# Performance work log

Measured on AMD Instinct MI355X. Metric: run time of the kernel, lower is better.

The kernel has to match this reference:

```python
import jax, jax.numpy as jnp
import numpy as np

HEAD_DIM = 128
N_HEADS = 32
N_KV = 8
EPS = 1e-6


def setup_inputs() -> dict:
    key = jax.random.key(0)
    ks = jax.random.split(key, 8)
    B, S, H = 1, 2048, 2560
    hidden_states = jax.random.normal(ks[0], (B, S, H), dtype=jnp.float32)
    # rotary embeddings (any values work for a math reference)
    pos = jnp.arange(S, dtype=jnp.float32)[:, None]
    inv_freq = 1.0 / (10000.0 ** (jnp.arange(0, HEAD_DIM, 2, dtype=jnp.float32) / HEAD_DIM))
    ang = pos * inv_freq[None, :]            # [S, HEAD_DIM/2]
    emb = jnp.concatenate([ang, ang], axis=-1)  # [S, HEAD_DIM]
    cos = jnp.cos(emb)[None]                 # [1, S, HEAD_DIM]
    sin = jnp.sin(emb)[None]
    sc = 0.02
    Wq = jax.random.normal(ks[1], (N_HEADS * HEAD_DIM, H), dtype=jnp.float32) * sc
    Wk = jax.random.normal(ks[2], (N_KV * HEAD_DIM, H), dtype=jnp.float32) * sc
    Wv = jax.random.normal(ks[3], (N_KV * HEAD_DIM, H), dtype=jnp.float32) * sc
    Wo = jax.random.normal(ks[4], (H, N_HEADS * HEAD_DIM), dtype=jnp.float32) * sc
    q_norm_w = jnp.ones((HEAD_DIM,), dtype=jnp.float32)
    k_norm_w = jnp.ones((HEAD_DIM,), dtype=jnp.float32)
    return dict(hidden_states=hidden_states, cos=cos, sin=sin,
                Wq=Wq, Wk=Wk, Wv=Wv, Wo=Wo,
                q_norm_w=q_norm_w, k_norm_w=k_norm_w)


def _rms_norm(x, w):
    var = jnp.mean(x * x, axis=-1, keepdims=True)
    return x * jax.lax.rsqrt(var + EPS) * w


def _rotate_half(x):
    x1, x2 = jnp.split(x, 2, axis=-1)
    return jnp.concatenate([-x2, x1], axis=-1)


def reference(hidden_states, cos, sin, Wq, Wk, Wv, Wo, q_norm_w, k_norm_w):
    B, S, H = hidden_states.shape
    scale = HEAD_DIM ** -0.5
    # projections -> [B, heads, S, D]
    q = (hidden_states @ Wq.T).reshape(B, S, N_HEADS, HEAD_DIM)
    k = (hidden_states @ Wk.T).reshape(B, S, N_KV, HEAD_DIM)
    v = (hidden_states @ Wv.T).reshape(B, S, N_KV, HEAD_DIM)
    q = _rms_norm(q, q_norm_w).transpose(0, 2, 1, 3)   # [B, 32, S, D]
    k = _rms_norm(k, k_norm_w).transpose(0, 2, 1, 3)   # [B, 8, S, D]
    v = v.transpose(0, 2, 1, 3)
    # RoPE (cos/sin broadcast over heads via [:, None])
    c = cos[:, None]
    s = sin[:, None]
    q = q * c + _rotate_half(q) * s
    k = k * c + _rotate_half(k) * s
    # GQA: expand kv heads (repeat_kv)
    rep = N_HEADS // N_KV
    k = jnp.repeat(k, rep, axis=1)  # [B, 32, S, D]
    v = jnp.repeat(v, rep, axis=1)
    # causal SDPA (prefill => is_causal=True, full-length cache)
    scores = jnp.einsum('bhqd,bhkd->bhqk', q, k) * scale
    causal = jnp.tril(jnp.ones((S, S), dtype=bool))
    scores = jnp.where(causal, scores, jnp.finfo(scores.dtype).min)
    probs = jax.nn.softmax(scores, axis=-1)
    out = jnp.einsum('bhqk,bhkd->bhqd', probs, v)      # [B, 32, S, D]
    out = out.transpose(0, 2, 1, 3).reshape(B, S, N_HEADS * HEAD_DIM)
    return out @ Wo.T
```

## Files before the change

### kernel.cpp

```cpp
#include <hip/hip_runtime.h>
#include <hip/hip_bf16.h>

#define S_LEN   2048
#define HID     2560
#define NH      32
#define NKV     8
#define HD      128
#define QDIM    (NH*HD)
#define KVDIM   (NKV*HD)

typedef __attribute__((ext_vector_type(8))) short short8;
typedef __attribute__((ext_vector_type(4))) float f32x4;

__device__ __forceinline__ unsigned short f2bf(float f) {
    unsigned u = __float_as_uint(f);
    u += 0x7fffu + ((u >> 16) & 1u);
    return (unsigned short)(u >> 16);
}
__device__ __forceinline__ float bf2f(unsigned short s) {
    return __uint_as_float(((unsigned)s) << 16);
}
__device__ __forceinline__ unsigned pk2bf(float a, float b) {
    __hip_bfloat162 h = __float22bfloat162_rn(make_float2(a, b));
    union { __hip_bfloat162 h; unsigned u; } c; c.h = h; return c.u;
}
__device__ __forceinline__ void gload16(const void* g, void* l) {
    __builtin_amdgcn_global_load_lds(
        (const __attribute__((address_space(1))) unsigned int*)g,
        (__attribute__((address_space(3))) unsigned int*)l, 16, 0, 0);
}

#define N4_HS  (S_LEN*HID/4)
#define N4_WQ  (QDIM*HID/4)
#define N4_WKV (KVDIM*HID/4)
__global__ __launch_bounds__(256) void cvt4(
    const float* __restrict__ hs, const float* __restrict__ Wq,
    const float* __restrict__ Wk, const float* __restrict__ Wv,
    unsigned short* __restrict__ hsB, unsigned short* __restrict__ WqB,
    unsigned short* __restrict__ WkB, unsigned short* __restrict__ WvB)
{
    int i = blockIdx.x * 256 + threadIdx.x;
    const float* s; unsigned short* d;
    if (i < N4_HS)                          { s = hs; d = hsB; }
    else if (i < N4_HS + N4_WQ)             { i -= N4_HS; s = Wq; d = WqB; }
    else if (i < N4_HS + N4_WQ + N4_WKV)    { i -= N4_HS + N4_WQ; s = Wk; d = WkB; }
    else                                    { i -= N4_HS + N4_WQ + N4_WKV; s = Wv; d = WvB; }
    float4 v = ((const float4*)s)[i];
    uint2 o;
    o.x = pk2bf(v.x, v.y); o.y = pk2bf(v.z, v.w);
    ((uint2*)d)[i] = o;
}

__global__ __launch_bounds__(256) void cvt_f32_bf16(
    const float* __restrict__ s, unsigned short* __restrict__ d, int n4)
{
    int i = blockIdx.x * 256 + threadIdx.x;
    if (i >= n4) return;
    float4 v = ((const float4*)s)[i];
    uint2 o;
    o.x = pk2bf(v.x, v.y); o.y = pk2bf(v.z, v.w);
    ((uint2*)d)[i] = o;
}

struct GemmRegs {
    f32x4 acc[4][4];
};
__device__ __forceinline__ void gemm_core(
    const unsigned short* A, const unsigned short* B, int Kd,
    unsigned short* As, unsigned short* Bs, GemmRegs& R,
    int rowA0, int rowB0, int tid)
{
    const int lane = tid & 63;
    const int l15 = lane & 15, l4 = lane >> 4;
    const int w = tid >> 6;
    const int wr = (w >> 1) * 64, wc = (w & 1) * 64;
    const int sw = l15 & 7;

#pragma unroll
    for (int i = 0; i < 4; i++)
#pragma unroll
        for (int j = 0; j < 4; j++)
            R.acc[i][j] = (f32x4){0.f, 0.f, 0.f, 0.f};

    for (int k0 = 0; k0 < Kd; k0 += 64) {
        __syncthreads();
#pragma unroll
        for (int i = 0; i < 4; i++) {
            int tc = tid + i * 256;
            int r = tc >> 3, cl = tc & 7;
            int cg = cl ^ (r & 7);
            gload16(A + (size_t)(rowA0 + r) * Kd + k0 + cg * 8, &As[tc * 8]);
            gload16(B + (size_t)(rowB0 + r) * Kd + k0 + cg * 8, &Bs[tc * 8]);
        }
        __syncthreads();

#pragma unroll
        for (int ks = 0; ks < 2; ks++) {
            const int kc = (ks * 4 + l4) ^ sw;
            short8 af[4], bf[4];
#pragma unroll
            for (int i = 0; i < 4; i++)
                af[i] = *(const short8*)&As[(wr + i*16 + l15)*64 + kc*8];
#pragma unroll
            for (int j = 0; j < 4; j++)
                bf[j] = *(const short8*)&Bs[(wc + j*16 + l15)*64 + kc*8];
#pragma unroll
            for (int i = 0; i < 4; i++)
#pragma unroll
                for (int j = 0; j < 4; j++)
                    R.acc[i][j] = __builtin_amdgcn_mfma_f32_16x16x32_bf16(
                        af[i], bf[j], R.acc[i][j], 0, 0, 0);
        }
    }
}

__global__ __launch_bounds__(256) void gemm_qkv(
    const unsigned short* __restrict__ A,
    const unsigned short* __restrict__ Wq, const unsigned short* __restrict__ Wk,
    const unsigned short* __restrict__ Wv,
    unsigned short* __restrict__ Qo, unsigned short* __restrict__ Ko,
    unsigned short* __restrict__ VTo)
{
    __shared__ unsigned short As[128*64];
    __shared__ unsigned short Bs[128*64];
    const int bx = blockIdx.x;
    const unsigned short* B;
    if (bx < 32)      B = Wq + (size_t)bx*128*HID;
    else if (bx < 40) B = Wk + (size_t)(bx-32)*128*HID;
    else              B = Wv + (size_t)(bx-40)*128*HID;

    const int tid = threadIdx.x;
    const int lane = tid & 63, w = tid >> 6;
    const int l15 = lane & 15, l4 = lane >> 4;
    const int wr = (w >> 1) * 64, wc = (w & 1) * 64;
    GemmRegs R;
    gemm_core(A, B, HID, As, Bs, R, blockIdx.y * 128, 0, tid);

    if (bx < 40) {
        unsigned short* C; int ldc, cb;
        if (bx < 32) { C = Qo; ldc = QDIM;  cb = bx*128; }
        else         { C = Ko; ldc = KVDIM; cb = (bx-32)*128; }
#pragma unroll
        for (int i = 0; i < 4; i++)
#pragma unroll
            for (int j = 0; j < 4; j++) {
                int row0 = blockIdx.y*128 + wr + i*16 + l4*4;
                int col  = cb + wc + j*16 + l15;
#pragma unroll
                for (int r = 0; r < 4; r++)
                    C[(size_t)(row0 + r) * ldc + col] = f2bf(R.acc[i][j][r]);
            }
    } else {
        const int cbase = (bx - 40) * 128;
#pragma unroll
        for (int i = 0; i < 4; i++)
#pragma unroll
            for (int j = 0; j < 4; j++) {
                int col  = cbase + wc + j*16 + l15;
                int row0 = blockIdx.y*128 + wr + i*16 + l4*4;
                int kvhh = col >> 7, d = col & 127;
                unsigned short* p = VTo + (size_t)kvhh*HD*S_LEN + (size_t)d*S_LEN + row0;
                uint2 pk;
                pk.x = pk2bf(R.acc[i][j][0], R.acc[i][j][1]);
                pk.y = pk2bf(R.acc[i][j][2], R.acc[i][j][3]);
                *(uint2*)p = pk;
            }
    }
}

__global__ __launch_bounds__(256) void gemm_out(
    const unsigned short* __restrict__ A, const unsigned short* __restrict__ B,
    float* __restrict__ C, int N, int Kd)
{
    __shared__ unsigned short As[64*64];
    __shared__ unsigned short Bs[160*64];
    const int tid = threadIdx.x;
    const int lane = tid & 63, w = tid >> 6;
    const int l15 = lane & 15, l4 = lane >> 4;
    const int wr = (w >> 1) * 32, wc = (w & 1) * 80;
    const int rowA0 = blockIdx.y * 64, rowB0 = blockIdx.x * 160;
    const int sw = l15 & 7;

    f32x4 acc[2][5];
#pragma unroll
    for (int i = 0; i < 2; i++)
#pragma unroll
        for (int j = 0; j < 5; j++) acc[i][j] = (f32x4){0.f, 0.f, 0.f, 0.f};

    for (int k0 = 0; k0 < Kd; k0 += 64) {
        __syncthreads();
#pragma unroll
        for (int i = 0; i < 2; i++) {
            int tc = tid + i * 256;
            int r = tc >> 3, cl = tc & 7;
            int cg = cl ^ (r & 7);
            gload16(A + (size_t)(rowA0 + r) * Kd + k0 + cg * 8, &As[tc * 8]);
        }
#pragma unroll
        for (int i = 0; i < 5; i++) {
            int tc = tid + i * 256;
            int r = tc >> 3, cl = tc & 7;
            int cg = cl ^ (r & 7);
            gload16(B + (size_t)(rowB0 + r) * Kd + k0 + cg * 8, &Bs[tc * 8]);
        }
        __syncthreads();

#pragma unroll
        for (int ks = 0; ks < 2; ks++) {
            const int kc = (ks * 4 + l4) ^ sw;
            short8 af[2], bf[5];
#pragma unroll
            for (int i = 0; i < 2; i++)
                af[i] = *(const short8*)&As[(wr + i*16 + l15)*64 + kc*8];
#pragma unroll
            for (int j = 0; j < 5; j++)
                bf[j] = *(const short8*)&Bs[(wc + j*16 + l15)*64 + kc*8];
#pragma unroll
            for (int i = 0; i < 2; i++)
#pragma unroll
                for (int j = 0; j < 5; j++)
                    acc[i][j] = __builtin_amdgcn_mfma_f32_16x16x32_bf16(
                        af[i], bf[j], acc[i][j], 0, 0, 0);
        }
    }

#pragma unroll
    for (int i = 0; i < 2; i++)
#pragma unroll
        for (int j = 0; j < 5; j++) {
            int row0 = rowA0 + wr + i*16 + l4*4;
            int col  = rowB0 + wc + j*16 + l15;
#pragma unroll
            for (int r = 0; r < 4; r++)
                C[(size_t)(row0 + r) * N + col] = acc[i][j][r];
        }
}

__global__ __launch_bounds__(256) void rmsnorm_rope_all(
    unsigned short* __restrict__ Qx, unsigned short* __restrict__ Kx,
    const float* __restrict__ qw, const float* __restrict__ kw,
    const float* __restrict__ ct, const float* __restrict__ st)
{
    int wid  = (blockIdx.x * blockDim.x + threadIdx.x) >> 6;
    int lane = threadIdx.x & 63;
    unsigned short* x; const float* w; int s;
    if (wid < S_LEN * NH) {
        int h = wid & (NH - 1); s = wid >> 5;
        x = Qx + (size_t)s * QDIM + h * HD; w = qw;
    } else {
        wid -= S_LEN * NH;
        int h = wid & (NKV - 1); s = wid >> 3;
        x = Kx + (size_t)s * KVDIM + h * HD; w = kw;
    }

    float x1 = bf2f(x[lane]);
    float x2 = bf2f(x[lane + 64]);
    float ss = x1*x1 + x2*x2;
#pragma unroll
    for (int off = 32; off > 0; off >>= 1) ss += __shfl_xor(ss, off, 64);
    float r = rsqrtf(ss * (1.0f/128.0f) + 1e-6f);
    float n1 = x1 * r * w[lane];
    float n2 = x2 * r * w[lane + 64];
    float c1 = ct[s*HD + lane],      s1 = st[s*HD + lane];
    float c2 = ct[s*HD + lane + 64], s2 = st[s*HD + lane + 64];
    x[lane]      = f2bf(n1*c1 - n2*s1);
    x[lane + 64] = f2bf(n2*c2 + n1*s2);
}

__global__ __launch_bounds__(256, 3) void flash_mfma(
    const unsigned short* __restrict__ Q, const unsigned short* __restrict__ K,
    const unsigned short* __restrict__ VT, unsigned short* __restrict__ O)
{
    const int bid = blockIdx.x;
    const int kvh = bid & 7;
    const int h   = kvh * 4 + ((bid >> 3) & 3);
    const int pb  = bid >> 5;
    const int tid = threadIdx.x;
    const int w = tid >> 6, lane = tid & 63;
    const int l15 = lane & 15, l4 = lane >> 4;

    __shared__ unsigned short Ks[64*128];
    __shared__ unsigned short Vt[128*64];
    __shared__ unsigned short Ps[4*16*72];
    __shared__ float Lw[4][16];

    const float scale2 = 0.08838834764831845f * 1.4426950408889634f;
    const float M2 = 17.3f;
    unsigned short* Pw = &Ps[w * 16 * 72];
    const unsigned short* VTh = VT + (size_t)kvh * HD * S_LEN;

#pragma unroll 1
    for (int phase = 0; phase < 2; phase++) {
        const int qt = phase ? pb : (31 - pb);
        const int q0 = qt * 64;

        short8 qa[4];
        {
            const unsigned short* qg = Q + (size_t)(q0 + w*16 + l15) * QDIM + h * HD;
#pragma unroll
            for (int ka = 0; ka < 4; ka++)
                qa[ka] = *(const short8*)(qg + ka*32 + l4*8);
        }

        const f32x4 zero = {0.f, 0.f, 0.f, 0.f};
        f32x4 accO[8];
#pragma unroll
        for (int j = 0; j < 8; j++) accO[j] = zero;
        float lsum = 0.f;

        for (int t = 0; t <= qt; t++) {
            const int c0 = t * 64;
            __syncthreads();
            {
#pragma unroll
                for (int i = 0; i < 4; i++) {
                    int tc = tid + i * 256;
                    int r = tc >> 4, cl = tc & 15;
                    int cg = cl ^ (r & 7);
                    gload16(K + (size_t)(c0 + r) * KVDIM + kvh * HD + cg * 8,
                            &Ks[tc * 8]);
                }
            }
            {
#pragma unroll
                for (int i = 0; i < 4; i++) {
                    int tc = tid + i * 256;
                    int r = tc >> 3, cl = tc & 7;
                    int cg = cl ^ (r & 7);
                    gload16(VTh + (size_t)r * S_LEN + c0 + cg * 8, &Vt[tc * 8]);
                }
            }
            __syncthreads();

            f32x4 sc[4];
#pragma unroll
            for (int mt = 0; mt < 4; mt++) sc[mt] = zero;
#pragma unroll
            for (int ka = 0; ka < 4; ka++) {
#pragma unroll
                for (int mt = 0; mt < 4; mt++) {
                    int row = mt*16 + l15;
                    int cs = (ka*4 + l4) ^ (row & 7);
                    short8 kb = *(const short8*)&Ks[row*128 + cs*8];
                    sc[mt] = __builtin_amdgcn_mfma_f32_16x16x32_bf16(kb, qa[ka], sc[mt], 0, 0, 0);
                }
            }

            const int qglob = q0 + w*16 + l15;
            const bool diag = (t == qt);
#pragma unroll
            for (int mt = 0; mt < 4; mt++) {
                float pv[4];
#pragma unroll
                for (int r = 0; r < 4; r++) {
                    int kvg = c0 + mt*16 + l4*4 + r;
                    float e = __builtin_amdgcn_exp2f(fmaf(sc[mt][r], scale2, -M2));
                    pv[r] = (!diag || kvg <= qglob) ? e : 0.f;
                    lsum += pv[r];
                }
                uint2 pk;
                pk.x = pk2bf(pv[0], pv[1]);
                pk.y = pk2bf(pv[2], pv[3]);
                *(uint2*)&Pw[l15*72 + mt*16 + l4*4] = pk;
            }

#pragma unroll
            for (int ks = 0; ks < 2; ks++) {
                short8 pf = *(const short8*)&Pw[l15*72 + ks*32 + l4*8];
                const int cs = (ks*4 + l4) ^ (l15 & 7);
#pragma unroll
                for (int dt = 0; dt < 8; dt++) {
                    short8 vf = *(const short8*)&Vt[(dt*16 + l15)*64 + cs*8];
                    accO[dt] = __builtin_amdgcn_mfma_f32_16x16x32_bf16(pf, vf, accO[dt], 0, 0, 0);
                }
            }
        }

        lsum += __shfl_xor(lsum, 16, 64);
        lsum += __shfl_xor(lsum, 32, 64);
        if (l4 == 0) Lw[w][l15] = lsum;
        f32x4 linv;
#pragma unroll
        for (int r = 0; r < 4; r++) linv[r] = 1.0f / Lw[w][l4*4 + r];

#pragma unroll
        for (int dt = 0; dt < 8; dt++)
#pragma unroll
            for (int r = 0; r < 4; r++) {
                int row_l = w*16 + l4*4 + r;
                O[(size_t)(q0 + row_l) * QDIM + h*HD + dt*16 + l15] =
                    f2bf(accO[dt][r] * linv[r]);
            }
    }
}

extern "C" void kernel_launch(void* const* d_in, const int* in_sizes, int n_in,
                              void* d_out, int out_size, void* d_ws, size_t ws_size,
                              hipStream_t stream)
{
    const float* hs   = (const float*)d_in[0];
    const float* cosb = (const float*)d_in[1];
    const float* sinb = (const float*)d_in[2];
    const float* Wq   = (const float*)d_in[3];
    const float* Wk   = (const float*)d_in[4];
    const float* Wv   = (const float*)d_in[5];
    const float* Wo   = (const float*)d_in[6];
    const float* qw   = (const float*)d_in[7];
    const float* kw   = (const float*)d_in[8];
    float* out = (float*)d_out;

    char* ws = (char*)d_ws;
    unsigned short* hsB = (unsigned short*)(ws);
    unsigned short* WqB = (unsigned short*)(ws + 10485760);
    unsigned short* WkB = (unsigned short*)(ws + 31457280);
    unsigned short* WvB = (unsigned short*)(ws + 36700160);
    unsigned short* KB  = (unsigned short*)(ws + 41943040);
    unsigned short* VT  = (unsigned short*)(ws + 46137344);
    unsigned short* WoB = (unsigned short*)(ws + 41943040);
    unsigned short* QB  = (unsigned short*)(ws + 62914560);
    unsigned short* CB  = (unsigned short*)(ws + 18874368);

    {
        int n4 = N4_HS + N4_WQ + 2 * N4_WKV;
        cvt4<<<(n4+255)/256, 256, 0, stream>>>(hs, Wq, Wk, Wv, hsB, WqB, WkB, WvB);
    }

    gemm_qkv<<<dim3(48, S_LEN/128), 256, 0, stream>>>(hsB, WqB, WkB, WvB, QB, KB, VT);

    rmsnorm_rope_all<<<S_LEN*(NH+NKV)/4, 256, 0, stream>>>(QB, KB, qw, kw, cosb, sinb);

    flash_mfma<<<512, 256, 0, stream>>>(QB, KB, VT, CB);

    cvt_f32_bf16<<<(HID*QDIM/4+255)/256, 256, 0, stream>>>(Wo, WoB, HID*QDIM/4);

    gemm_out<<<dim3(HID/160, S_LEN/64), 256, 0, stream>>>(CB, WoB, out, HID, QDIM);
}
```

Before: 365.4 us.

## Load two KV tiles per barrier pair in flash attention loop

The flash attention inner loop now stages two 64-row K/V tiles into separate shared buffers between one pair of barriers, then computes both, with a tail for odd tile counts. This halves the number of __syncthreads and issues more global loads in flight per stage. Shared memory doubles and launch bounds drop from 3 to 2 blocks per CU, reducing occupancy. There is still no overlap between loads and compute.

```diff
diff --git a/kernel.cpp b/kernel.cpp
--- a/kernel.cpp
+++ b/kernel.cpp
@@ -267,7 +267,71 @@
     x[lane + 64] = f2bf(n2*c2 + n1*s2);
 }
 
-__global__ __launch_bounds__(256, 3) void flash_mfma(
+#define FSTG_K(t_, b_) do {                                                  \
+    int c0_ = (t_) * 64;                                                     \
+    _Pragma("unroll")                                                        \
+    for (int i_ = 0; i_ < 4; i_++) {                                         \
+        int tc_ = tid + i_ * 256;                                            \
+        int r_ = tc_ >> 4, cl_ = tc_ & 15;                                   \
+        int cg_ = cl_ ^ (r_ & 7);                                            \
+        gload16(K + (size_t)(c0_ + r_) * KVDIM + kvh * HD + cg_ * 8,         \
+                &Ks[b_][tc_ * 8]);                                           \
+    } } while (0)
+
+#define FSTG_V(t_, b_) do {                                                  \
+    int c0_ = (t_) * 64;                                                     \
+    _Pragma("unroll")                                                        \
+    for (int i_ = 0; i_ < 4; i_++) {                                         \
+        int tc_ = tid + i_ * 256;                                            \
+        int r_ = tc_ >> 3, cl_ = tc_ & 7;                                    \
+        int cg_ = cl_ ^ (r_ & 7);                                            \
+        gload16(VTh + (size_t)r_ * S_LEN + c0_ + cg_ * 8,                    \
+                &Vt[b_][tc_ * 8]);                                           \
+    } } while (0)
+
+#define FCOMP(t_, B_) do {                                                   \
+    const int c0_ = (t_) * 64;                                               \
+    f32x4 sc[4];                                                             \
+    _Pragma("unroll")                                                        \
+    for (int mt = 0; mt < 4; mt++) sc[mt] = zero;                            \
+    _Pragma("unroll")                                                        \
+    for (int ka = 0; ka < 4; ka++) {                                         \
+        _Pragma("unroll")                                                    \
+        for (int mt = 0; mt < 4; mt++) {                                     \
+            int row = mt*16 + l15;                                           \
+            int cs = (ka*4 + l4) ^ (row & 7);                                \
+            short8 kb = *(const short8*)&Ks[B_][row*128 + cs*8];             \
+            sc[mt] = __builtin_amdgcn_mfma_f32_16x16x32_bf16(kb, qa[ka], sc[mt], 0, 0, 0); \
+        }                                                                    \
+    }                                                                        \
+    const bool diag = ((t_) == qt);                                          \
+    _Pragma("unroll")                                                        \
+    for (int mt = 0; mt < 4; mt++) {                                         \
+        float pv[4];                                                         \
+        _Pragma("unroll")                                                    \
+        for (int r = 0; r < 4; r++) {                                        \
+            int kvg = c0_ + mt*16 + l4*4 + r;                                \
+            float e = __builtin_amdgcn_exp2f(fmaf(sc[mt][r], scale2, -M2));  \
+            pv[r] = (!diag || kvg <= qglob) ? e : 0.f;                       \
+            lsum += pv[r];                                                   \
+        }                                                                    \
+        uint2 pk;                                                            \
+        pk.x = pk2bf(pv[0], pv[1]);                                          \
+        pk.y = pk2bf(pv[2], pv[3]);                                          \
+        *(uint2*)&Pw[l15*72 + mt*16 + l4*4] = pk;                            \
+    }                                                                        \
+    _Pragma("unroll")                                                        \
+    for (int ks = 0; ks < 2; ks++) {                                         \
+        short8 pf = *(const short8*)&Pw[l15*72 + ks*32 + l4*8];              \
+        const int cs = (ks*4 + l4) ^ (l15 & 7);                              \
+        _Pragma("unroll")                                                    \
+        for (int dt = 0; dt < 8; dt++) {                                     \
+            short8 vf = *(const short8*)&Vt[B_][(dt*16 + l15)*64 + cs*8];    \
+            accO[dt] = __builtin_amdgcn_mfma_f32_16x16x32_bf16(pf, vf, accO[dt], 0, 0, 0); \
+        }                                                                    \
+    } } while (0)
+
+__global__ __launch_bounds__(256, 2) void flash_mfma(
     const unsigned short* __restrict__ Q, const unsigned short* __restrict__ K,
     const unsigned short* __restrict__ VT, unsigned short* __restrict__ O)
 {
@@ -279,8 +343,8 @@
     const int w = tid >> 6, lane = tid & 63;
     const int l15 = lane & 15, l4 = lane >> 4;
 
-    __shared__ unsigned short Ks[64*128];
-    __shared__ unsigned short Vt[128*64];
+    __shared__ unsigned short Ks[2][64*128];
+    __shared__ unsigned short Vt[2][128*64];
     __shared__ unsigned short Ps[4*16*72];
     __shared__ float Lw[4][16];
 
@@ -307,73 +371,22 @@
 #pragma unroll
         for (int j = 0; j < 8; j++) accO[j] = zero;
         float lsum = 0.f;
-
-        for (int t = 0; t <= qt; t++) {
-            const int c0 = t * 64;
+        const int qglob = q0 + w*16 + l15;
+
+        int t = 0;
+        for (; t + 1 <= qt; t += 2) {
             __syncthreads();
-            {
-#pragma unroll
-                for (int i = 0; i < 4; i++) {
-                    int tc = tid + i * 256;
-                    int r = tc >> 4, cl = tc & 15;
-                    int cg = cl ^ (r & 7);
-                    gload16(K + (size_t)(c0 + r) * KVDIM + kvh * HD + cg * 8,
-                            &Ks[tc * 8]);
-                }
-            }
-            {
-#pragma unroll
-                for (int i = 0; i < 4; i++) {
-                    int tc = tid + i * 256;
-                    int r = tc >> 3, cl = tc & 7;
-                    int cg = cl ^ (r & 7);
-                    gload16(VTh + (size_t)r * S_LEN + c0 + cg * 8, &Vt[tc * 8]);
-                }
-            }
+            FSTG_K(t, 0); FSTG_V(t, 0);
+            FSTG_K(t + 1, 1); FSTG_V(t + 1, 1);
             __syncthreads();
-
-            f32x4 sc[4];
-#pragma unroll
-            for (int mt = 0; mt < 4; mt++) sc[mt] = zero;
-#pragma unroll
-            for (int ka = 0; ka < 4; ka++) {
-#pragma unroll
-                for (int mt = 0; mt < 4; mt++) {
-                    int row = mt*16 + l15;
-                    int cs = (ka*4 + l4) ^ (row & 7);
-                    short8 kb = *(const short8*)&Ks[row*128 + cs*8];
-                    sc[mt] = __builtin_amdgcn_mfma_f32_16x16x32_bf16(kb, qa[ka], sc[mt], 0, 0, 0);
-                }
-            }
-
-            const int qglob = q0 + w*16 + l15;
-            const bool diag = (t == qt);
-#pragma unroll
-            for (int mt = 0; mt < 4; mt++) {
-                float pv[4];
-#pragma unroll
-                for (int r = 0; r < 4; r++) {
-                    int kvg = c0 + mt*16 + l4*4 + r;
-                    float e = __builtin_amdgcn_exp2f(fmaf(sc[mt][r], scale2, -M2));
-                    pv[r] = (!diag || kvg <= qglob) ? e : 0.f;
-                    lsum += pv[r];
-                }
-                uint2 pk;
-                pk.x = pk2bf(pv[0], pv[1]);
-                pk.y = pk2bf(pv[2], pv[3]);
-                *(uint2*)&Pw[l15*72 + mt*16 + l4*4] = pk;
-            }
-
-#pragma unroll
-            for (int ks = 0; ks < 2; ks++) {
-                short8 pf = *(const short8*)&Pw[l15*72 + ks*32 + l4*8];
-                const int cs = (ks*4 + l4) ^ (l15 & 7);
-#pragma unroll
-                for (int dt = 0; dt < 8; dt++) {
-                    short8 vf = *(const short8*)&Vt[(dt*16 + l15)*64 + cs*8];
-                    accO[dt] = __builtin_amdgcn_mfma_f32_16x16x32_bf16(pf, vf, accO[dt], 0, 0, 0);
-                }
-            }
+            FCOMP(t, 0);
+            FCOMP(t + 1, 1);
+        }
+        if (t <= qt) {
+            __syncthreads();
+            FSTG_K(t, 0); FSTG_V(t, 0);
+            __syncthreads();
+            FCOMP(t, 0);
         }
 
         lsum += __shfl_xor(lsum, 16, 64);
```

Result: no change. 362.6 us (-0.8%).
